# Performance work log

Measured on AMD Instinct MI355X. Metric: run time of the kernel, lower is better.

The kernel has to match this reference:

```python
import jax, jax.numpy as jnp
import numpy as np

B, T1, T2 = 4, 768, 256
T = T1 + T2            # n_token
NI = T2                # n_i_token
D = 1024               # n_embd
H_MLP = 4096           # n_mlp_hidden
L = 12                 # n_layer
V = 512                # num_class / vocab_size
EPS = 1e-5


def _ln(x, g, b):
    m = jnp.mean(x, axis=-1, keepdims=True)
    v = jnp.mean((x - m) ** 2, axis=-1, keepdims=True)
    return (x - m) * jax.lax.rsqrt(v + EPS) * g + b


def setup_inputs() -> dict:
    key = jax.random.key(0)
    ks = jax.random.split(key, 16)
    s = 0.02
    return {
        "xt": jax.random.randint(ks[0], (B, T1), 0, V, dtype=jnp.int32),
        "zi": jax.random.randint(ks[1], (B, T2), 0, V, dtype=jnp.int32),
        "pos_emb": jax.random.normal(ks[2], (T, D), jnp.float32) * s,
        "t_emb": jax.random.normal(ks[3], (V, D), jnp.float32) * s,
        "i_emb": jax.random.normal(ks[4], (V, D), jnp.float32) * s,
        "ln1_g": jnp.ones((L, D), jnp.float32),
        "ln1_b": jnp.zeros((L, D), jnp.float32),
        "Wq": jax.random.normal(ks[5], (L, D, D), jnp.float32) * s,
        "Wk": jax.random.normal(ks[6], (L, D, D), jnp.float32) * s,
        "Wv": jax.random.normal(ks[7], (L, D, D), jnp.float32) * s,
        "ln2_g": jnp.ones((L, D), jnp.float32),
        "ln2_b": jnp.zeros((L, D), jnp.float32),
        "W1": jax.random.normal(ks[8], (L, D, H_MLP), jnp.float32) * s,
        "b1": jnp.zeros((L, H_MLP), jnp.float32),
        "W2": jax.random.normal(ks[9], (L, H_MLP, D), jnp.float32) * s,
        "b2": jnp.zeros((L, D), jnp.float32),
        "ro_W": jax.random.normal(ks[10], (D, V), jnp.float32) * s,
        "ro_b": jnp.zeros((V,), jnp.float32),
    }


def reference(xt, zi, pos_emb, t_emb, i_emb, ln1_g, ln1_b, Wq, Wk, Wv,
              ln2_g, ln2_b, W1, b1, W2, b2, ro_W, ro_b):
    # token + position embeddings: [B, T, D]
    H0 = jnp.concatenate([i_emb[zi], t_emb[xt]], axis=1) + pos_emb[None]
    scale = 1.0 / np.sqrt(D).astype(np.float32)

    def layer(H, p):
        g1, b1_, wq, wk, wv, g2, b2_, w1, bb1, w2, bb2 = p
        H1 = _ln(H, g1, b1_)
        q = H1 @ wq  # [B, T, D]
        k = H1 @ wk
        v = H1 @ wv
        attn = jax.nn.softmax(jnp.einsum('bid,bjd->bij', q, k) * scale, axis=-1)
        H = H + jnp.einsum('bij,bjd->bid', attn, v)
        # second application with extra rescale by embedding dim (H.shape[2] == D)
        H = H + jnp.einsum('bij,bjd->bid', attn / D, v)
        H2 = _ln(H, g2, b2_)
        H = H + jax.nn.gelu(H2 @ w1 + bb1, approximate=False) @ w2 + bb2
        return H, None

    params = (ln1_g, ln1_b, Wq, Wk, Wv, ln2_g, ln2_b, W1, b1, W2, b2)
    H, _ = jax.lax.scan(layer, H0, params)
    prediction = H @ ro_W + ro_b  # [B, T, V]
    return prediction[:, NI:, :]
```

## Files before the change

### kernel.cpp

```cpp
#include <hip/hip_runtime.h>
#include <hip/hip_bf16.h>
#include <math.h>

#define D_EMB  1024
#define T_TOK  1024
#define T1_TOK 768
#define T2_TOK 256
#define HMLP   4096
#define NLAYER 12
#define VCLS   512

typedef __attribute__((ext_vector_type(8))) short          short8;
typedef __attribute__((ext_vector_type(4))) float          f32x4;
typedef __attribute__((ext_vector_type(4))) unsigned short us4;
typedef unsigned short us;

__device__ __forceinline__ us f2bf(float f) {
    union { float f; unsigned int u; } c; c.f = f;
    unsigned int u = c.u;
    return (us)((u + 0x7FFFu + ((u >> 16) & 1u)) >> 16);
}

__device__ __forceinline__ void gld_lds16(const us* g, us* l) {
    __builtin_amdgcn_global_load_lds(
        (__attribute__((address_space(1))) void*)g,
        (__attribute__((address_space(3))) void*)l, 16, 0, 0);
}

__global__ __launch_bounds__(256)
void embed_kernel(const int* __restrict__ xt, const int* __restrict__ zi,
                  const float* __restrict__ pos, const float* __restrict__ temb,
                  const float* __restrict__ iemb, float* __restrict__ H)
{
    const long idx = (long)blockIdx.x * 256 + threadIdx.x;
    const long e   = idx * 4;
    const int  dd  = (int)(e & (D_EMB - 1));
    const long bt  = e >> 10;
    const int  t   = (int)(bt & (T_TOK - 1));
    const int  b   = (int)(bt >> 10);
    const float* src;
    if (t < T2_TOK) src = iemb + (long)zi[b * T2_TOK + t] * D_EMB + dd;
    else            src = temb + (long)xt[b * T1_TOK + (t - T2_TOK)] * D_EMB + dd;
    float4 sv = *(const float4*)src;
    float4 pv = *(const float4*)(pos + (long)t * D_EMB + dd);
    float4 o; o.x = sv.x + pv.x; o.y = sv.y + pv.y; o.z = sv.z + pv.z; o.w = sv.w + pv.w;
    *(float4*)(H + e) = o;
}

__global__ __launch_bounds__(256)
void ln_kernel(const float* __restrict__ X, const float* __restrict__ g,
               const float* __restrict__ b, us* __restrict__ Y)
{
    const long row = blockIdx.x;
    const int  tid = threadIdx.x;
    float4 v = *(const float4*)(X + row * D_EMB + tid * 4);
    float s = v.x + v.y + v.z + v.w;
    float q = v.x*v.x + v.y*v.y + v.z*v.z + v.w*v.w;
    #pragma unroll
    for (int o = 32; o >= 1; o >>= 1) { s += __shfl_down(s, o); q += __shfl_down(q, o); }
    __shared__ float rs[4], rq[4];
    const int w = tid >> 6;
    if ((tid & 63) == 0) { rs[w] = s; rq[w] = q; }
    __syncthreads();
    s = rs[0] + rs[1] + rs[2] + rs[3];
    q = rq[0] + rq[1] + rq[2] + rq[3];
    const float mean = s * (1.0f / D_EMB);
    const float var  = q * (1.0f / D_EMB) - mean * mean;
    const float rstd = rsqrtf(var + 1e-5f);
    float4 gg = *(const float4*)(g + tid * 4);
    float4 bb = *(const float4*)(b + tid * 4);
    us4 o;
    o.x = f2bf((v.x - mean) * rstd * gg.x + bb.x);
    o.y = f2bf((v.y - mean) * rstd * gg.y + bb.y);
    o.z = f2bf((v.z - mean) * rstd * gg.z + bb.z);
    o.w = f2bf((v.w - mean) * rstd * gg.w + bb.w);
    *(us4*)(Y + row * D_EMB + tid * 4) = o;
}

__global__ __launch_bounds__(256)
void softmax_kernel(const float* __restrict__ S, us* __restrict__ P)
{
    const long row = blockIdx.x;
    const int  tid = threadIdx.x;
    float4 v = *(const float4*)(S + row * T_TOK + tid * 4);
    const float sc = 0.03125f;
    float a = v.x * sc, b = v.y * sc, c = v.z * sc, d = v.w * sc;
    float mx = fmaxf(fmaxf(a, b), fmaxf(c, d));
    #pragma unroll
    for (int o = 32; o >= 1; o >>= 1) mx = fmaxf(mx, __shfl_down(mx, o));
    __shared__ float rm[4], rsum[4];
    const int w = tid >> 6;
    if ((tid & 63) == 0) rm[w] = mx;
    __syncthreads();
    mx = fmaxf(fmaxf(rm[0], rm[1]), fmaxf(rm[2], rm[3]));
    float e0 = expf(a - mx), e1 = expf(b - mx), e2 = expf(c - mx), e3 = expf(d - mx);
    float s = e0 + e1 + e2 + e3;
    #pragma unroll
    for (int o = 32; o >= 1; o >>= 1) s += __shfl_down(s, o);
    if ((tid & 63) == 0) rsum[w] = s;
    __syncthreads();
    s = rsum[0] + rsum[1] + rsum[2] + rsum[3];
    const float inv = 1.0f / s;
    us4 o4; o4.x = f2bf(e0 * inv); o4.y = f2bf(e1 * inv);
    o4.z = f2bf(e2 * inv); o4.w = f2bf(e3 * inv);
    *(us4*)(P + row * T_TOK + tid * 4) = o4;
}

__global__ __launch_bounds__(256)
void convT_kernel(const float* __restrict__ src, us* __restrict__ dst,
                  int K, int N)
{
    __shared__ us tile[32][33];
    const int tn = blockIdx.x, tk = blockIdx.y;
    const int tx = threadIdx.x & 31, ty = threadIdx.x >> 5;
    #pragma unroll
    for (int i = 0; i < 4; ++i) {
        const int r = ty + i * 8;
        tile[r][tx] = f2bf(src[(long)(tk * 32 + r) * N + tn * 32 + tx]);
    }
    __syncthreads();
    #pragma unroll
    for (int i = 0; i < 4; ++i) {
        const int r = ty + i * 8;
        dst[(long)(tn * 32 + r) * K + tk * 32 + tx] = tile[tx][r];
    }
}

__global__ __launch_bounds__(256)
void wconv_kernel(const float* __restrict__ Wq, const float* __restrict__ Wk,
                  const float* __restrict__ Wv, const float* __restrict__ W1,
                  const float* __restrict__ W2,
                  us* __restrict__ WqT, us* __restrict__ WkT,
                  us* __restrict__ WvT, us* __restrict__ W1T,
                  us* __restrict__ W2T)
{
    __shared__ us tile[64][66];
    const int t = blockIdx.x;
    const float* src; us* dst; int K, N, tk, tn;
    if (t < 768) {
        const int wsel = t >> 8, tt = t & 255;
        src = (wsel == 0) ? Wq : (wsel == 1) ? Wk : Wv;
        dst = (wsel == 0) ? WqT : (wsel == 1) ? WkT : WvT;
        K = 1024; N = 1024; tk = tt >> 4; tn = tt & 15;
    } else if (t < 1792) {
        const int tt = t - 768;
        src = W1; dst = W1T; K = 1024; N = 4096; tk = tt >> 6; tn = tt & 63;
    } else {
        const int tt = t - 1792;
        src = W2; dst = W2T; K = 4096; N = 1024; tk = tt >> 4; tn = tt & 15;
    }
    const int r  = threadIdx.x >> 4;
    const int c4 = threadIdx.x & 15;
    #pragma unroll
    for (int i = 0; i < 4; ++i) {
        const int row = r + i * 16;
        float4 v = *(const float4*)(src + (long)(tk * 64 + row) * N + tn * 64 + c4 * 4);
        tile[row][c4 * 4 + 0] = f2bf(v.x);
        tile[row][c4 * 4 + 1] = f2bf(v.y);
        tile[row][c4 * 4 + 2] = f2bf(v.z);
        tile[row][c4 * 4 + 3] = f2bf(v.w);
    }
    __syncthreads();
    #pragma unroll
    for (int i = 0; i < 4; ++i) {
        const int rr = r + i * 16;
        us4 o;
        o.x = tile[c4 * 4 + 0][rr];
        o.y = tile[c4 * 4 + 1][rr];
        o.z = tile[c4 * 4 + 2][rr];
        o.w = tile[c4 * 4 + 3][rr];
        *(us4*)(dst + (long)(tn * 64 + rr) * K + tk * 64 + c4 * 4) = o;
    }
}

__global__ __launch_bounds__(256)
void cvt_bf16_kernel(const float* __restrict__ X, us* __restrict__ Y)
{
    const long i = ((long)blockIdx.x * 256 + threadIdx.x) * 4;
    float4 v = *(const float4*)(X + i);
    us4 o; o.x = f2bf(v.x); o.y = f2bf(v.y); o.z = f2bf(v.z); o.w = f2bf(v.w);
    *(us4*)(Y + i) = o;
}

template<int EPI>
__global__ __launch_bounds__(512, 2)
void gemm8(const us* __restrict__ A, const us* __restrict__ B,
           void* __restrict__ C0, void* __restrict__ C1, void* __restrict__ C2,
           const float* __restrict__ bias,
           int N, int K, int kLen)
{
    constexpr int ABUF = 256 * 64;
    constexpr int BBUF = 128 * 64;
    __shared__ us As[3 * ABUF];
    __shared__ us Bs[3 * BBUF];

    const int z = blockIdx.z;
    const int kOff = (kLen < K) ? z * kLen : 0;

    const int gx = gridDim.x, gy = gridDim.y;
    const int o  = blockIdx.x + gx * blockIdx.y;
    const int nwg = gx * gy;
    const int virt = (nwg & 7) ? o : ((o & 7) * (nwg >> 3) + (o >> 3));
    const int ntile = virt / gy;
    const int mtile = virt - ntile * gy;
    const int m0 = mtile * 256, n0 = ntile * 128;

    const int tid  = threadIdx.x;
    const int lane = tid & 63, w = tid >> 6;
    const int srow = lane >> 3, sslot = (lane & 7) ^ srow;
    const int lr = lane & 15, hi = lane >> 4;
    const int wm = (w >> 1) * 64, wn = (w & 1) * 64;

    const us* gA = A + (long)(m0 + w * 32 + srow) * K + kOff + sslot * 8;
    const us* gB = B + (long)(n0 + w * 16 + srow) * K + kOff + sslot * 8;

    f32x4 acc[4][4];
    #pragma unroll
    for (int f = 0; f < 4; ++f)
        #pragma unroll
        for (int g = 0; g < 4; ++g)
            acc[f][g] = (f32x4){0.f, 0.f, 0.f, 0.f};

    const int nk = kLen >> 6;

    #pragma unroll
    for (int j = 0; j < 4; ++j)
        gld_lds16(gA + (long)(j * 8) * K + 0, As + 0 * ABUF + (w * 32 + j * 8) * 64);
    #pragma unroll
    for (int j = 0; j < 2; ++j)
        gld_lds16(gB + (long)(j * 8) * K + 0, Bs + 0 * BBUF + (w * 16 + j * 8) * 64);
    #pragma unroll
    for (int j = 0; j < 4; ++j)
        gld_lds16(gA + (long)(j * 8) * K + 64, As + 1 * ABUF + (w * 32 + j * 8) * 64);
    #pragma unroll
    for (int j = 0; j < 2; ++j)
        gld_lds16(gB + (long)(j * 8) * K + 64, Bs + 1 * BBUF + (w * 16 + j * 8) * 64);
    asm volatile("s_waitcnt vmcnt(6)" ::: "memory");
    __builtin_amdgcn_s_barrier();

    for (int t = 0; t < nk; ++t) {
        const int cur = t % 3, nb = (t + 2) % 3;
        const us* Ac = As + cur * ABUF;
        const us* Bc = Bs + cur * BBUF;
        const int kk2 = (t + 2) << 6;
        #pragma unroll
        for (int kk = 0; kk < 2; ++kk) {
            short8 af[4], bg[4];
            #pragma unroll
            for (int f = 0; f < 4; ++f) {
                const int rr = wm + f * 16 + lr;
                af[f] = *(const short8*)&Ac[rr * 64 + (((kk * 4 + hi) ^ (rr & 7)) * 8)];
            }
            #pragma unroll
            for (int g = 0; g < 4; ++g) {
                const int rn = wn + g * 16 + lr;
                bg[g] = *(const short8*)&Bc[rn * 64 + (((kk * 4 + hi) ^ (rn & 7)) * 8)];
            }
            if (t + 2 < nk) {
                gld_lds16(gA + (long)((kk * 2 + 0) * 8) * K + kk2,
                          As + nb * ABUF + (w * 32 + (kk * 2 + 0) * 8) * 64);
                gld_lds16(gA + (long)((kk * 2 + 1) * 8) * K + kk2,
                          As + nb * ABUF + (w * 32 + (kk * 2 + 1) * 8) * 64);
                gld_lds16(gB + (long)(kk * 8) * K + kk2,
                          Bs + nb * BBUF + (w * 16 + kk * 8) * 64);
            }
            __builtin_amdgcn_s_barrier();
            asm volatile("s_waitcnt lgkmcnt(0)" ::: "memory");
            __builtin_amdgcn_sched_barrier(0);
            __builtin_amdgcn_s_setprio(1);
            #pragma unroll
            for (int f = 0; f < 4; ++f)
                #pragma unroll
                for (int g = 0; g < 4; ++g)
                    acc[f][g] = __builtin_amdgcn_mfma_f32_16x16x32_bf16(
                        af[f], bg[g], acc[f][g], 0, 0, 0);
            __builtin_amdgcn_s_setprio(0);
            __builtin_amdgcn_sched_barrier(0);
            if (kk == 1) {
                if (t + 2 < nk)      asm volatile("s_waitcnt vmcnt(6)" ::: "memory");
                else if (t + 1 < nk) asm volatile("s_waitcnt vmcnt(0)" ::: "memory");
            }
            __builtin_amdgcn_s_barrier();
        }
    }

    #pragma unroll
    for (int f = 0; f < 4; ++f) {
        #pragma unroll
        for (int g = 0; g < 4; ++g) {
            const int gm0 = m0 + wm + f * 16 + hi * 4;
            const int gn  = n0 + wn + g * 16 + lr;
            if constexpr (EPI == 7) {
                const int target = gn >> 10, col = gn & 1023;
                if (target == 2) {
                    us4 ov;
                    ov.x = f2bf(acc[f][g][0]); ov.y = f2bf(acc[f][g][1]);
                    ov.z = f2bf(acc[f][g][2]); ov.w = f2bf(acc[f][g][3]);
                    *(us4*)&((us*)C2)[(long)(gm0 >> 10) * (T_TOK * D_EMB)
                                      + (long)col * T_TOK + (gm0 & (T_TOK - 1))] = ov;
                } else {
                    us* dst = target ? (us*)C1 : (us*)C0;
                    #pragma unroll
                    for (int r = 0; r < 4; ++r)
                        dst[(long)(gm0 + r) * D_EMB + col] = f2bf(acc[f][g][r]);
                }
            } else if constexpr (EPI == 1) {
                #pragma unroll
                for (int r = 0; r < 4; ++r) {
                    float v = acc[f][g][r] + bias[gn];
                    const float ge = 0.5f * v * (1.0f + erff(v * 0.70710678118f));
                    ((us*)C0)[(long)(gm0 + r) * N + gn] = f2bf(ge);
                }
            } else {
                #pragma unroll
                for (int r = 0; r < 4; ++r)
                    atomicAdd((float*)C0 + (long)(gm0 + r) * N + gn,
                              acc[f][g][r] + ((z == 0) ? bias[gn] : 0.f));
            }
        }
    }
}

template<int EPI, int TN>
__global__ __launch_bounds__(256)
void gemm_bt(const us* __restrict__ A, const us* __restrict__ B0,
             void* __restrict__ C0, const float* __restrict__ bias,
             int M, int N, int K,
             long sAz, long sBz, long sCz, float alpha)
{
    constexpr int FN = TN / 32;
    constexpr int ABUF = 128 * 32;
    constexpr int BBUF = TN * 32;
    __shared__ us As[2 * ABUF];
    __shared__ us Bs[2 * BBUF];

    const int z = blockIdx.z;
    const us* Ap = A + (long)z * sAz;
    const us* Bp = B0 + (long)z * sBz;
    const long czoff = (long)z * sCz;

    const int gx = gridDim.x, gy = gridDim.y;
    const int o  = blockIdx.x + gx * blockIdx.y;
    const int nwg = gx * gy;
    const int virt = (nwg & 7) ? o : ((o & 7) * (nwg >> 3) + (o >> 3));
    const int ntile = virt / gy;
    int mtile = virt - ntile * gy;
    if constexpr (EPI == 4) mtile = (mtile / 6) * 8 + 2 + (mtile % 6);
    const int m0 = mtile * 128, n0 = ntile * TN;

    const int tid = threadIdx.x;
    const int l = tid & 63, w = tid >> 6;
    const int wm = (w >> 1) * 64, wn = (w & 1) * (TN / 2);
    const int lr = l & 15, hi = l >> 4;

    const int r0 = tid >> 2;
    const int s0 = (tid & 3) ^ ((r0 >> 1) & 3);
    const us* gA0 = Ap + (long)(m0 + r0) * K + s0 * 8;
    const us* gA1 = Ap + (long)(m0 + r0 + 64) * K + s0 * 8;
    const us* gB0 = Bp + (long)(n0 + r0) * K + s0 * 8;
    const us* gB1 = (TN == 128) ? Bp + (long)(n0 + r0 + 64) * K + s0 * 8 : nullptr;
    const int lA0 = w * 512, lA1 = 2048 + w * 512;
    const int lB0 = w * 512, lB1 = 2048 + w * 512;

    f32x4 acc[4][FN];
    #pragma unroll
    for (int f = 0; f < 4; ++f)
        #pragma unroll
        for (int gq = 0; gq < FN; ++gq)
            acc[f][gq] = (f32x4){0.f, 0.f, 0.f, 0.f};

    const int nk = K >> 5;
    gld_lds16(gA0, As + lA0);
    gld_lds16(gA1, As + lA1);
    gld_lds16(gB0, Bs + lB0);
    if constexpr (TN == 128) gld_lds16(gB1, Bs + lB1);
    __syncthreads();

    for (int t = 0; t < nk; ++t) {
        const int cur = t & 1;
        const int aB = (cur ^ 1) * ABUF, bB = (cur ^ 1) * BBUF;
        if (t + 1 < nk) {
            const int k1 = (t + 1) << 5;
            gld_lds16(gA0 + k1, As + aB + lA0);
            gld_lds16(gA1 + k1, As + aB + lA1);
            gld_lds16(gB0 + k1, Bs + bB + lB0);
            if constexpr (TN == 128) gld_lds16(gB1 + k1, Bs + bB + lB1);
        }
        const int aC = cur * ABUF, bC = cur * BBUF;
        short8 af[4], bg[FN];
        #pragma unroll
        for (int f = 0; f < 4; ++f) {
            const int rr = wm + f * 16 + lr;
            const int sl = hi ^ ((rr >> 1) & 3);
            af[f] = *(const short8*)&As[aC + rr * 32 + sl * 8];
        }
        #pragma unroll
        for (int gq = 0; gq < FN; ++gq) {
            const int rn = wn + gq * 16 + lr;
            const int sl = hi ^ ((rn >> 1) & 3);
            bg[gq] = *(const short8*)&Bs[bC + rn * 32 + sl * 8];
        }
        #pragma unroll
        for (int f = 0; f < 4; ++f)
            #pragma unroll
            for (int gq = 0; gq < FN; ++gq)
                acc[f][gq] = __builtin_amdgcn_mfma_f32_16x16x32_bf16(
                    af[f], bg[gq], acc[f][gq], 0, 0, 0);
        __syncthreads();
    }

    #pragma unroll
    for (int f = 0; f < 4; ++f) {
        #pragma unroll
        for (int gq = 0; gq < FN; ++gq) {
            #pragma unroll
            for (int r = 0; r < 4; ++r) {
                const int gm = m0 + wm + f * 16 + hi * 4 + r;
                const int gn = n0 + wn + gq * 16 + lr;
                float v = acc[f][gq][r];
                if constexpr (EPI == 0) {
                    ((float*)C0)[czoff + (long)gm * N + gn] = v;
                } else if constexpr (EPI == 3) {
                    float* c = (float*)C0 + czoff + (long)gm * N + gn;
                    *c = *c + alpha * v;
                } else {
                    const int tt = gm & (T_TOK - 1);
                    ((float*)C0)[(long)((gm >> 10) * T1_TOK + (tt - T2_TOK)) * VCLS + gn]
                        = v + bias[gn];
                }
            }
        }
    }
}

extern "C" void kernel_launch(void* const* d_in, const int* in_sizes, int n_in,
                              void* d_out, int out_size, void* d_ws, size_t ws_size,
                              hipStream_t stream)
{
    (void)in_sizes; (void)n_in; (void)out_size; (void)ws_size;
    const int*   xt   = (const int*)d_in[0];
    const int*   zi   = (const int*)d_in[1];
    const float* pos  = (const float*)d_in[2];
    const float* temb = (const float*)d_in[3];
    const float* iemb = (const float*)d_in[4];
    const float* ln1g = (const float*)d_in[5];
    const float* ln1b = (const float*)d_in[6];
    const float* Wq   = (const float*)d_in[7];
    const float* Wk   = (const float*)d_in[8];
    const float* Wv   = (const float*)d_in[9];
    const float* ln2g = (const float*)d_in[10];
    const float* ln2b = (const float*)d_in[11];
    const float* W1   = (const float*)d_in[12];
    const float* b1   = (const float*)d_in[13];
    const float* W2   = (const float*)d_in[14];
    const float* b2   = (const float*)d_in[15];
    const float* roW  = (const float*)d_in[16];
    const float* rob  = (const float*)d_in[17];
    float* out = (float*)d_out;

    char* wsb = (char*)d_ws;
    float* H    = (float*)(wsb + 0);
    us*    LNb  = (us*)(wsb + 16777216);
    float* S    = (float*)(wsb + 25165824);
    us*    Qb   = (us*)(wsb + 41943040);
    us*    Kb   = (us*)(wsb + 50331648);
    us*    VT   = (us*)(wsb + 58720256);
    us*    Pb   = (us*)(wsb + 67108864);
    us*    Hid  = (us*)(wsb + 41943040);
    us*    WqT  = (us*)(wsb + 75497472);
    us*    WkT  = (us*)(wsb + 77594624);
    us*    WvT  = (us*)(wsb + 79691776);
    us*    W1T  = (us*)(wsb + 81788928);
    us*    W2T  = (us*)(wsb + 90177536);
    us*    roWT = W1T;
    us*    Hbf  = LNb;

    const long TD = (long)T_TOK * D_EMB;
    const long TT = (long)T_TOK * T_TOK;

    embed_kernel<<<4096, 256, 0, stream>>>(xt, zi, pos, temb, iemb, H);

    for (int lyr = 0; lyr < NLAYER; ++lyr) {
        const long dd = (long)lyr * D_EMB * D_EMB;
        const long d1 = (long)lyr * D_EMB * HMLP;
        wconv_kernel<<<2816, 256, 0, stream>>>(
            Wq + dd, Wk + dd, Wv + dd, W1 + d1, W2 + d1,
            WqT, WkT, WvT, W1T, W2T);
        ln_kernel<<<4096, 256, 0, stream>>>(H, ln1g + lyr * D_EMB, ln1b + lyr * D_EMB, LNb);
        gemm8<7><<<dim3(24, 16, 1), 512, 0, stream>>>(
            LNb, WqT, Qb, Kb, VT, nullptr, 3072, D_EMB, D_EMB);
        gemm_bt<0, 64><<<dim3(16, 8, 4), 256, 0, stream>>>(
            Qb, Kb, S, nullptr, T_TOK, T_TOK, D_EMB, TD, TD, TT, 1.f);
        softmax_kernel<<<4096, 256, 0, stream>>>(S, Pb);
        gemm_bt<3, 64><<<dim3(16, 8, 4), 256, 0, stream>>>(
            Pb, VT, H, nullptr, T_TOK, D_EMB, T_TOK, TT, TD, TD,
            1.0f + 1.0f / (float)D_EMB);
        ln_kernel<<<4096, 256, 0, stream>>>(H, ln2g + lyr * D_EMB, ln2b + lyr * D_EMB, LNb);
        gemm8<1><<<dim3(32, 16, 1), 512, 0, stream>>>(
            LNb, W1T, Hid, nullptr, nullptr, b1 + (long)lyr * HMLP,
            HMLP, D_EMB, D_EMB);
        gemm8<6><<<dim3(8, 16, 2), 512, 0, stream>>>(
            Hid, W2T, H, nullptr, nullptr, b2 + (long)lyr * D_EMB,
            D_EMB, HMLP, HMLP / 2);
    }
    cvt_bf16_kernel<<<4096, 256, 0, stream>>>(H, Hbf);
    convT_kernel<<<dim3(16, 32), 256, 0, stream>>>(roW, roWT, D_EMB, VCLS);
    gemm_bt<4, 64><<<dim3(8, 24, 1), 256, 0, stream>>>(
        Hbf, roWT, out, rob, 4096, VCLS, D_EMB, 0L, 0L, 0L, 1.f);
}
```

Before: 3.053 ms.

## Route attention and MLP-down GEMMs through templated 256x64 gemm8 kernel

Generalizes gemm8 with a TN template (64 or 128 column tiles) and a per-batch B stride chosen from the M tile. It then uses this kernel for the QKV projection, QK^T scores, PV accumulation, and the W2 down-projection. The W2 GEMM drops split-K with float atomics in favour of a plain read-modify-write epilogue. The goal is larger, better-pipelined tiles and no atomic traffic, at the cost of fewer K-parallel workgroups and smaller N tiles for some GEMMs.

```diff
diff --git a/kernel.cpp b/kernel.cpp
--- a/kernel.cpp
+++ b/kernel.cpp
@@ -182,20 +182,19 @@
     *(us4*)(Y + i) = o;
 }
 
-template<int EPI>
+template<int EPI, int TN>
 __global__ __launch_bounds__(512, 2)
 void gemm8(const us* __restrict__ A, const us* __restrict__ B,
            void* __restrict__ C0, void* __restrict__ C1, void* __restrict__ C2,
            const float* __restrict__ bias,
-           int N, int K, int kLen)
-{
+           int N, int K, long sBz, float alpha)
+{
+    constexpr int FN   = TN / 32;
     constexpr int ABUF = 256 * 64;
-    constexpr int BBUF = 128 * 64;
+    constexpr int BBUF = TN * 64;
+    constexpr int BROW = (TN == 128) ? 16 : 8;
     __shared__ us As[3 * ABUF];
     __shared__ us Bs[3 * BBUF];
-
-    const int z = blockIdx.z;
-    const int kOff = (kLen < K) ? z * kLen : 0;
 
     const int gx = gridDim.x, gy = gridDim.y;
     const int o  = blockIdx.x + gx * blockIdx.y;
@@ -203,39 +202,45 @@
     const int virt = (nwg & 7) ? o : ((o & 7) * (nwg >> 3) + (o >> 3));
     const int ntile = virt / gy;
     const int mtile = virt - ntile * gy;
-    const int m0 = mtile * 256, n0 = ntile * 128;
+    const int m0 = mtile * 256, n0 = ntile * TN;
+
+    const us* Bp = B + (long)(m0 >> 10) * sBz;
 
     const int tid  = threadIdx.x;
     const int lane = tid & 63, w = tid >> 6;
     const int srow = lane >> 3, sslot = (lane & 7) ^ srow;
     const int lr = lane & 15, hi = lane >> 4;
-    const int wm = (w >> 1) * 64, wn = (w & 1) * 64;
-
-    const us* gA = A + (long)(m0 + w * 32 + srow) * K + kOff + sslot * 8;
-    const us* gB = B + (long)(n0 + w * 16 + srow) * K + kOff + sslot * 8;
-
-    f32x4 acc[4][4];
+    const int wm = (w >> 1) * 64, wn = (w & 1) * (TN / 2);
+
+    const us* gA = A + (long)(m0 + w * 32 + srow) * K + sslot * 8;
+    const us* gB = Bp + (long)(n0 + w * BROW + srow) * K + sslot * 8;
+
+    f32x4 acc[4][FN];
     #pragma unroll
     for (int f = 0; f < 4; ++f)
         #pragma unroll
-        for (int g = 0; g < 4; ++g)
+        for (int g = 0; g < FN; ++g)
             acc[f][g] = (f32x4){0.f, 0.f, 0.f, 0.f};
 
-    const int nk = kLen >> 6;
-
-    #pragma unroll
-    for (int j = 0; j < 4; ++j)
-        gld_lds16(gA + (long)(j * 8) * K + 0, As + 0 * ABUF + (w * 32 + j * 8) * 64);
-    #pragma unroll
-    for (int j = 0; j < 2; ++j)
-        gld_lds16(gB + (long)(j * 8) * K + 0, Bs + 0 * BBUF + (w * 16 + j * 8) * 64);
-    #pragma unroll
-    for (int j = 0; j < 4; ++j)
-        gld_lds16(gA + (long)(j * 8) * K + 64, As + 1 * ABUF + (w * 32 + j * 8) * 64);
-    #pragma unroll
-    for (int j = 0; j < 2; ++j)
-        gld_lds16(gB + (long)(j * 8) * K + 64, Bs + 1 * BBUF + (w * 16 + j * 8) * 64);
-    asm volatile("s_waitcnt vmcnt(6)" ::: "memory");
+    const int nk = K >> 6;
+
+    #pragma unroll
+    for (int tb = 0; tb < 2; ++tb) {
+        #pragma unroll
+        for (int j = 0; j < 4; ++j)
+            gld_lds16(gA + (long)(j * 8) * K + tb * 64,
+                      As + tb * ABUF + (w * 32 + j * 8) * 64);
+        if constexpr (TN == 128) {
+            #pragma unroll
+            for (int j = 0; j < 2; ++j)
+                gld_lds16(gB + (long)(j * 8) * K + tb * 64,
+                          Bs + tb * BBUF + (w * 16 + j * 8) * 64);
+        } else {
+            gld_lds16(gB + tb * 64, Bs + tb * BBUF + (w * 8) * 64);
+        }
+    }
+    if constexpr (TN == 128) asm volatile("s_waitcnt vmcnt(6)" ::: "memory");
+    else                     asm volatile("s_waitcnt vmcnt(5)" ::: "memory");
     __builtin_amdgcn_s_barrier();
 
     for (int t = 0; t < nk; ++t) {
@@ -245,14 +250,14 @@
         const int kk2 = (t + 2) << 6;
         #pragma unroll
         for (int kk = 0; kk < 2; ++kk) {
-            short8 af[4], bg[4];
+            short8 af[4], bg[FN];
             #pragma unroll
             for (int f = 0; f < 4; ++f) {
                 const int rr = wm + f * 16 + lr;
                 af[f] = *(const short8*)&Ac[rr * 64 + (((kk * 4 + hi) ^ (rr & 7)) * 8)];
             }
             #pragma unroll
-            for (int g = 0; g < 4; ++g) {
+            for (int g = 0; g < FN; ++g) {
                 const int rn = wn + g * 16 + lr;
                 bg[g] = *(const short8*)&Bc[rn * 64 + (((kk * 4 + hi) ^ (rn & 7)) * 8)];
             }
@@ -261,8 +266,12 @@
                           As + nb * ABUF + (w * 32 + (kk * 2 + 0) * 8) * 64);
                 gld_lds16(gA + (long)((kk * 2 + 1) * 8) * K + kk2,
                           As + nb * ABUF + (w * 32 + (kk * 2 + 1) * 8) * 64);
-                gld_lds16(gB + (long)(kk * 8) * K + kk2,
-                          Bs + nb * BBUF + (w * 16 + kk * 8) * 64);
+                if constexpr (TN == 128) {
+                    gld_lds16(gB + (long)(kk * 8) * K + kk2,
+                              Bs + nb * BBUF + (w * 16 + kk * 8) * 64);
+                } else if (kk == 0) {
+                    gld_lds16(gB + kk2, Bs + nb * BBUF + (w * 8) * 64);
+                }
             }
             __builtin_amdgcn_s_barrier();
             asm volatile("s_waitcnt lgkmcnt(0)" ::: "memory");
@@ -271,14 +280,20 @@
             #pragma unroll
             for (int f = 0; f < 4; ++f)
                 #pragma unroll
-                for (int g = 0; g < 4; ++g)
+                for (int g = 0; g < FN; ++g)
                     acc[f][g] = __builtin_amdgcn_mfma_f32_16x16x32_bf16(
                         af[f], bg[g], acc[f][g], 0, 0, 0);
             __builtin_amdgcn_s_setprio(0);
             __builtin_amdgcn_sched_barrier(0);
             if (kk == 1) {
-                if (t + 2 < nk)      asm volatile("s_waitcnt vmcnt(6)" ::: "memory");
-                else if (t + 1 < nk) asm volatile("s_waitcnt vmcnt(0)" ::: "memory");
+                if (t + 2 < nk) {
+                    if constexpr (TN == 128)
+                        asm volatile("s_waitcnt vmcnt(6)" ::: "memory");
+                    else
+                        asm volatile("s_waitcnt vmcnt(5)" ::: "memory");
+                } else if (t + 1 < nk) {
+                    asm volatile("s_waitcnt vmcnt(0)" ::: "memory");
+                }
             }
             __builtin_amdgcn_s_barrier();
         }
@@ -287,7 +302,7 @@
     #pragma unroll
     for (int f = 0; f < 4; ++f) {
         #pragma unroll
-        for (int g = 0; g < 4; ++g) {
+        for (int g = 0; g < FN; ++g) {
             const int gm0 = m0 + wm + f * 16 + hi * 4;
             const int gn  = n0 + wn + g * 16 + lr;
             if constexpr (EPI == 7) {
@@ -311,11 +326,22 @@
                     const float ge = 0.5f * v * (1.0f + erff(v * 0.70710678118f));
                     ((us*)C0)[(long)(gm0 + r) * N + gn] = f2bf(ge);
                 }
+            } else if constexpr (EPI == 0) {
+                #pragma unroll
+                for (int r = 0; r < 4; ++r)
+                    ((float*)C0)[(long)(gm0 + r) * N + gn] = acc[f][g][r];
+            } else if constexpr (EPI == 2) {
+                #pragma unroll
+                for (int r = 0; r < 4; ++r) {
+                    float* c = (float*)C0 + (long)(gm0 + r) * N + gn;
+                    *c = *c + acc[f][g][r] + bias[gn];
+                }
             } else {
                 #pragma unroll
-                for (int r = 0; r < 4; ++r)
-                    atomicAdd((float*)C0 + (long)(gm0 + r) * N + gn,
-                              acc[f][g][r] + ((z == 0) ? bias[gn] : 0.f));
+                for (int r = 0; r < 4; ++r) {
+                    float* c = (float*)C0 + (long)(gm0 + r) * N + gn;
+                    *c = *c + alpha * acc[f][g][r];
+                }
             }
         }
     }
@@ -334,10 +360,8 @@
     __shared__ us As[2 * ABUF];
     __shared__ us Bs[2 * BBUF];
 
-    const int z = blockIdx.z;
-    const us* Ap = A + (long)z * sAz;
-    const us* Bp = B0 + (long)z * sBz;
-    const long czoff = (long)z * sCz;
+    const us* Ap = A;
+    const us* Bp = B0;
 
     const int gx = gridDim.x, gy = gridDim.y;
     const int o  = blockIdx.x + gx * blockIdx.y;
@@ -358,9 +382,8 @@
     const us* gA0 = Ap + (long)(m0 + r0) * K + s0 * 8;
     const us* gA1 = Ap + (long)(m0 + r0 + 64) * K + s0 * 8;
     const us* gB0 = Bp + (long)(n0 + r0) * K + s0 * 8;
-    const us* gB1 = (TN == 128) ? Bp + (long)(n0 + r0 + 64) * K + s0 * 8 : nullptr;
     const int lA0 = w * 512, lA1 = 2048 + w * 512;
-    const int lB0 = w * 512, lB1 = 2048 + w * 512;
+    const int lB0 = w * 512;
 
     f32x4 acc[4][FN];
     #pragma unroll
@@ -373,7 +396,6 @@
     gld_lds16(gA0, As + lA0);
     gld_lds16(gA1, As + lA1);
     gld_lds16(gB0, Bs + lB0);
-    if constexpr (TN == 128) gld_lds16(gB1, Bs + lB1);
     __syncthreads();
 
     for (int t = 0; t < nk; ++t) {
@@ -384,7 +406,6 @@
             gld_lds16(gA0 + k1, As + aB + lA0);
             gld_lds16(gA1 + k1, As + aB + lA1);
             gld_lds16(gB0 + k1, Bs + bB + lB0);
-            if constexpr (TN == 128) gld_lds16(gB1 + k1, Bs + bB + lB1);
         }
         const int aC = cur * ABUF, bC = cur * BBUF;
         short8 af[4], bg[FN];
@@ -417,17 +438,9 @@
             for (int r = 0; r < 4; ++r) {
                 const int gm = m0 + wm + f * 16 + hi * 4 + r;
                 const int gn = n0 + wn + gq * 16 + lr;
-                float v = acc[f][gq][r];
-                if constexpr (EPI == 0) {
-                    ((float*)C0)[czoff + (long)gm * N + gn] = v;
-                } else if constexpr (EPI == 3) {
-                    float* c = (float*)C0 + czoff + (long)gm * N + gn;
-                    *c = *c + alpha * v;
-                } else {
-                    const int tt = gm & (T_TOK - 1);
-                    ((float*)C0)[(long)((gm >> 10) * T1_TOK + (tt - T2_TOK)) * VCLS + gn]
-                        = v + bias[gn];
-                }
+                const int tt = gm & (T_TOK - 1);
+                ((float*)C0)[(long)((gm >> 10) * T1_TOK + (tt - T2_TOK)) * VCLS + gn]
+                    = acc[f][gq][r] + bias[gn];
             }
         }
     }
@@ -476,7 +489,6 @@
     us*    Hbf  = LNb;
 
     const long TD = (long)T_TOK * D_EMB;
-    const long TT = (long)T_TOK * T_TOK;
 
     embed_kernel<<<4096, 256, 0, stream>>>(xt, zi, pos, temb, iemb, H);
 
@@ -487,21 +499,21 @@
             Wq + dd, Wk + dd, Wv + dd, W1 + d1, W2 + d1,
             WqT, WkT, WvT, W1T, W2T);
         ln_kernel<<<4096, 256, 0, stream>>>(H, ln1g + lyr * D_EMB, ln1b + lyr * D_EMB, LNb);
-        gemm8<7><<<dim3(24, 16, 1), 512, 0, stream>>>(
-            LNb, WqT, Qb, Kb, VT, nullptr, 3072, D_EMB, D_EMB);
-        gemm_bt<0, 64><<<dim3(16, 8, 4), 256, 0, stream>>>(
-            Qb, Kb, S, nullptr, T_TOK, T_TOK, D_EMB, TD, TD, TT, 1.f);
+        gemm8<7, 64><<<dim3(48, 16, 1), 512, 0, stream>>>(
+            LNb, WqT, Qb, Kb, VT, nullptr, 3072, D_EMB, 0L, 1.f);
+        gemm8<0, 64><<<dim3(16, 16, 1), 512, 0, stream>>>(
+            Qb, Kb, S, nullptr, nullptr, nullptr, T_TOK, D_EMB, TD, 1.f);
         softmax_kernel<<<4096, 256, 0, stream>>>(S, Pb);
-        gemm_bt<3, 64><<<dim3(16, 8, 4), 256, 0, stream>>>(
-            Pb, VT, H, nullptr, T_TOK, D_EMB, T_TOK, TT, TD, TD,
+        gemm8<3, 64><<<dim3(16, 16, 1), 512, 0, stream>>>(
+            Pb, VT, H, nullptr, nullptr, nullptr, D_EMB, T_TOK, TD,
             1.0f + 1.0f / (float)D_EMB);
         ln_kernel<<<4096, 256, 0, stream>>>(H, ln2g + lyr * D_EMB, ln2b + lyr * D_EMB, LNb);
-        gemm8<1><<<dim3(32, 16, 1), 512, 0, stream>>>(
+        gemm8<1, 128><<<dim3(32, 16, 1), 512, 0, stream>>>(
             LNb, W1T, Hid, nullptr, nullptr, b1 + (long)lyr * HMLP,
-            HMLP, D_EMB, D_EMB);
-        gemm8<6><<<dim3(8, 16, 2), 512, 0, stream>>>(
+            HMLP, D_EMB, 0L, 1.f);
+        gemm8<2, 64><<<dim3(16, 16, 1), 512, 0, stream>>>(
             Hid, W2T, H, nullptr, nullptr, b2 + (long)lyr * D_EMB,
-            D_EMB, HMLP, HMLP / 2);
+            D_EMB, HMLP, 0L, 1.f);
     }
     cvt_bf16_kernel<<<4096, 256, 0, stream>>>(H, Hbf);
     convT_kernel<<<dim3(16, 32), 256, 0, stream>>>(roW, roWT, D_EMB, VCLS);
```

Result: no change. 3.051 ms (-0.1%).
